# Kernel optimization log

Hardware: AMD Instinct MI355X
Metric: run time of the kernel (lower is better)

## Reference

```python
import jax, jax.numpy as jnp
import numpy as np

LN_EPS = 1e-5

# Per-tensor symmetric fake-quant (brevitas-style):
#  - activations: signed int8, non-narrow range [-128, 127], scale = absmax / 128
#  - weights:     signed int8, narrow range     [-127, 127], scale = absmax / 127

def _fake_quant(v, qmin, qmax, denom):
    s = jnp.max(jnp.abs(v)) / denom
    s = jnp.maximum(s, jnp.asarray(1e-12, v.dtype))
    q = jnp.clip(jnp.round(v / s), qmin, qmax)
    return q * s

def fq_act(v):
    return _fake_quant(v, -128.0, 127.0, 128.0)

def fq_weight(w):
    return _fake_quant(w, -127.0, 127.0, 127.0)

def layer_norm(x, gamma, beta):
    mu = jnp.mean(x, axis=-1, keepdims=True)
    var = jnp.mean(jnp.square(x - mu), axis=-1, keepdims=True)
    return (x - mu) * jax.lax.rsqrt(var + LN_EPS) * gamma + beta


def setup_inputs() -> dict:
    key = jax.random.key(0)
    k_x, k_w1, k_w2 = jax.random.split(key, 3)
    B, T, D, H = 16, 4096, 768, 3072
    x = jax.random.normal(k_x, (B, T, D), dtype=jnp.float32)
    gamma = jnp.ones((D,), jnp.float32)
    beta = jnp.zeros((D,), jnp.float32)
    W1 = jax.random.normal(k_w1, (H, D), dtype=jnp.float32) * (1.0 / np.sqrt(D))
    b1 = jnp.zeros((H,), jnp.float32)
    W2 = jax.random.normal(k_w2, (D, H), dtype=jnp.float32) * (1.0 / np.sqrt(H))
    b2 = jnp.zeros((D,), jnp.float32)
    return {"x": x, "gamma": gamma, "beta": beta, "W1": W1, "b1": b1, "W2": W2, "b2": b2}


def reference(x, gamma, beta, W1, b1, W2, b2):
    xn = layer_norm(x, gamma, beta)
    # fc1: quantize input + weight per-tensor, GEMM, float bias add
    h = jnp.einsum('btd,hd->bth', fq_act(xn), fq_weight(W1)) + b1
    h = jax.nn.gelu(h, approximate=False)  # nn.GELU default = exact erf
    # dropout p=0 -> identity
    out = jnp.einsum('bth,dh->btd', fq_act(h), fq_weight(W2)) + b2
    return out
```

## Files before the change

kernel.cpp:

```cpp
#include <hip/hip_runtime.h>
#include <math.h>


typedef __attribute__((ext_vector_type(4))) float  f4;
typedef __attribute__((ext_vector_type(4))) int    i32x4;
typedef __attribute__((ext_vector_type(4))) unsigned char  uc4;
typedef __attribute__((ext_vector_type(4))) unsigned int   u4;

__device__ __forceinline__ unsigned short f2bf_rn(float f) {
    unsigned u = __float_as_uint(f);
    u += 0x7FFFu + ((u >> 16) & 1u);
    return (unsigned short)(u >> 16);
}

template <int NW>
__device__ __forceinline__ void block_atomic_max(float v, unsigned* slot,
                                                 float* red, int tid) {
    int lane = tid & 63, wv = tid >> 6;
    #pragma unroll
    for (int m = 32; m; m >>= 1) v = fmaxf(v, __shfl_xor(v, m));
    if (lane == 0) red[wv] = v;
    __syncthreads();
    if (tid == 0) {
        float r = red[0];
        #pragma unroll
        for (int i = 1; i < NW; i++) r = fmaxf(r, red[i]);
        atomicMax(slot, __float_as_uint(r));
    }
}

__device__ __forceinline__ void gll16(const void* g, void* l) {
    __builtin_amdgcn_global_load_lds(
        (const __attribute__((address_space(1))) void*)g,
        (__attribute__((address_space(3))) void*)l, 16, 0, 0);
}

__device__ __forceinline__ void ln_row(const f4* xr, int lane, f4 v[3],
                                       float& mu, float& rs) {
    float s = 0.f;
    #pragma unroll
    for (int c = 0; c < 3; c++) {
        v[c] = xr[lane + 64 * c];
        s += v[c][0] + v[c][1] + v[c][2] + v[c][3];
    }
    #pragma unroll
    for (int m = 1; m < 64; m <<= 1) s += __shfl_xor(s, m);
    mu = s * (1.0f / 768.0f);
    float q = 0.f;
    #pragma unroll
    for (int c = 0; c < 3; c++) {
        #pragma unroll
        for (int k = 0; k < 4; k++) { float d = v[c][k] - mu; q += d * d; }
    }
    #pragma unroll
    for (int m = 1; m < 64; m <<= 1) q += __shfl_xor(q, m);
    rs = rsqrtf(q * (1.0f / 768.0f) + 1e-5f);
}

__global__ __launch_bounds__(256) void ln_absmax_kernel(
        const float* __restrict__ x, const float* __restrict__ gamma,
        const float* __restrict__ beta, unsigned* __restrict__ slot, long NR) {
    __shared__ float red[4];
    int tid = threadIdx.x, lane = tid & 63, wv = tid >> 6;
    const f4* g4 = (const f4*)gamma;
    const f4* b4 = (const f4*)beta;
    long rstep = (long)gridDim.x * 4;
    float wmax = 0.f;
    for (long row = (long)blockIdx.x * 4 + wv; row < NR; row += rstep) {
        const f4* xr = (const f4*)(x + row * 768);
        f4 v[3]; float mu, rs;
        ln_row(xr, lane, v, mu, rs);
        #pragma unroll
        for (int c = 0; c < 3; c++) {
            f4 g = g4[lane + 64 * c], b = b4[lane + 64 * c];
            #pragma unroll
            for (int k = 0; k < 4; k++) {
                float xn = (v[c][k] - mu) * rs * g[k] + b[k];
                wmax = fmaxf(wmax, fabsf(xn));
            }
        }
    }
    block_atomic_max<4>(wmax, slot, red, tid);
}

__global__ __launch_bounds__(256) void ln_quant_kernel(
        const float* __restrict__ x, const float* __restrict__ gamma,
        const float* __restrict__ beta, unsigned char* __restrict__ qx,
        const unsigned* __restrict__ amax_bits, long NR) {
    int tid = threadIdx.x, lane = tid & 63, wv = tid >> 6;
    long row = (long)blockIdx.x * 4 + wv;
    if (row >= NR) return;
    float sx = fmaxf(__uint_as_float(*amax_bits) * (1.0f / 128.0f), 1e-12f);
    const f4* xr = (const f4*)(x + row * 768);
    const f4* g4 = (const f4*)gamma;
    const f4* b4 = (const f4*)beta;
    f4 v[3]; float mu, rs;
    ln_row(xr, lane, v, mu, rs);
    uc4* qr = (uc4*)(qx + row * 768);
    #pragma unroll
    for (int c = 0; c < 3; c++) {
        f4 g = g4[lane + 64 * c], b = b4[lane + 64 * c];
        uc4 o;
        #pragma unroll
        for (int k = 0; k < 4; k++) {
            float xn = (v[c][k] - mu) * rs * g[k] + b[k];
            float q = fminf(fmaxf(rintf(xn / sx), -128.0f), 127.0f);
            o[k] = (unsigned char)(int)q;
        }
        qr[lane + 64 * c] = o;
    }
}

__global__ __launch_bounds__(256) void absmax_kernel(
        const float* __restrict__ w, long n4, unsigned* __restrict__ slot) {
    __shared__ float red[4];
    int tid = threadIdx.x;
    long stride = (long)gridDim.x * 256;
    float mx = 0.f;
    for (long i = (long)blockIdx.x * 256 + tid; i < n4; i += stride) {
        f4 v = ((const f4*)w)[i];
        mx = fmaxf(mx, fmaxf(fmaxf(fabsf(v[0]), fabsf(v[1])),
                             fmaxf(fabsf(v[2]), fabsf(v[3]))));
    }
    block_atomic_max<4>(mx, slot, red, tid);
}

__global__ __launch_bounds__(256) void quant_w_kernel(
        const float* __restrict__ w, unsigned char* __restrict__ qw, long n4,
        const unsigned* __restrict__ amax_bits) {
    long i = (long)blockIdx.x * 256 + threadIdx.x;
    if (i >= n4) return;
    float s = fmaxf(__uint_as_float(*amax_bits) * (1.0f / 127.0f), 1e-12f);
    f4 v = ((const f4*)w)[i];
    uc4 o;
    #pragma unroll
    for (int k = 0; k < 4; k++) {
        float q = fminf(fmaxf(rintf(v[k] / s), -127.0f), 127.0f);
        o[k] = (unsigned char)(int)q;
    }
    ((uc4*)qw)[i] = o;
}

__global__ __launch_bounds__(256) void quant_h_kernel(
        unsigned int* __restrict__ h, const unsigned* __restrict__ amax_bits,
        long n32) {
    long i = (long)blockIdx.x * 256 + threadIdx.x;
    if (i >= n32) return;
    float s = fmaxf(__uint_as_float(*amax_bits) * (1.0f / 128.0f), 1e-12f);
    u4 d0 = ((const u4*)h)[2 * i];
    u4 d1 = ((const u4*)h)[2 * i + 1];
    u4 o;
    #pragma unroll
    for (int w = 0; w < 4; w++) {
        unsigned r = 0;
        #pragma unroll
        for (int j = 0; j < 2; j++) {
            unsigned dw = (w < 2) ? d0[(w & 1) * 2 + j] : d1[(w & 1) * 2 + j];
            float lo = __uint_as_float(dw << 16);
            float hi = __uint_as_float(dw & 0xFFFF0000u);
            int qa = (int)fminf(fmaxf(rintf(lo / s), -128.0f), 127.0f);
            int qb = (int)fminf(fmaxf(rintf(hi / s), -128.0f), 127.0f);
            r |= ((unsigned)(unsigned char)qa) << (16 * j);
            r |= ((unsigned)(unsigned char)qb) << (16 * j + 8);
        }
        o[w] = r;
    }
    ((u4*)h)[2 * i] = o;
}

#define AB(b,kh) ((b)*65536 + (kh)*16384)
#define BB(b,kh) ((b)*65536 + 32768 + (kh)*16384)
#define VMC(n) asm volatile("s_waitcnt vmcnt(" #n ")" ::: "memory")
#define SK(eo, rbA, rbB) {                                                    \
    gll16(gA[0] + (long)(eo) * GAP, lds + (rbA) + ldst[0]);                   \
    gll16(gA[1] + (long)(eo) * GAP, lds + (rbA) + ldst[1]);                   \
    gll16(gB[0] + (eo),             lds + (rbB) + ldst[0]);                   \
    gll16(gB[1] + (eo),             lds + (rbB) + ldst[1]); }

#define PHASE2(BUF, KS, STAGE, TAIL) do {                                     \
    i32x4 aF[8]; i32x4 bF[4];                                                 \
    _Pragma("unroll")                                                         \
    for (int m_ = 0; m_ < 8; m_++)                                            \
      aF[m_] = *(const i32x4*)(lds + AB(BUF,KS) + aoff + m_ * 1024);          \
    _Pragma("unroll")                                                         \
    for (int n_ = 0; n_ < 4; n_++)                                            \
      bF[n_] = *(const i32x4*)(lds + BB(BUF,KS) + boff + n_ * 1024);          \
    STAGE                                                                     \
    __builtin_amdgcn_s_barrier();                                             \
    asm volatile("s_waitcnt lgkmcnt(0)" ::: "memory");                        \
    __builtin_amdgcn_s_setprio(1);                                            \
    _Pragma("unroll")                                                         \
    for (int m_ = 0; m_ < 8; m_++)                                            \
      _Pragma("unroll")                                                       \
      for (int n_ = 0; n_ < 4; n_++)                                          \
        acc[m_][n_] = __builtin_amdgcn_mfma_i32_16x16x64_i8(                  \
            aF[m_], bF[n_], acc[m_][n_], 0, 0, 0);                            \
    __builtin_amdgcn_s_setprio(0);                                            \
    TAIL                                                                      \
    __builtin_amdgcn_s_barrier();                                             \
  } while (0)

template <int GAP, int EPI>
__global__ __launch_bounds__(512, 2) void gemm256i(
        const unsigned char* __restrict__ A, const unsigned char* __restrict__ B,
        int K, const unsigned* __restrict__ amaxA_bits,
        const unsigned* __restrict__ amaxB_bits, const float* __restrict__ bias,
        void* __restrict__ Cout, int ldc, unsigned* __restrict__ amax_out) {
    __shared__ __align__(16) char lds[131072];
    __shared__ float red[8];
    int tid = threadIdx.x, lane = tid & 63, wv = tid >> 6;
    int wm = wv >> 2, wn = wv & 3;

    int nwg = gridDim.x * gridDim.y;
    int flat = blockIdx.y * gridDim.x + blockIdx.x;
    int swz = (flat & 7) * (nwg >> 3) + (flat >> 3);
    int ncol = gridDim.x;
    long rowBase = (long)(swz / ncol) * 256;
    long colBase = (long)(swz % ncol) * 256;

    i32x4 acc[8][4] = {};

    int rl = lane & 15, cq = lane >> 4;
    int roff = rl * 64 + ((cq ^ ((rl >> 1) & 3)) * 16);
    int aoff = wm * 8192 + roff;
    int boff = wn * 4096 + roff;

    const unsigned char* gA[2]; const unsigned char* gB[2]; int ldst[2];
    #pragma unroll
    for (int p = 0; p < 2; p++) {
        int s = p * 512 + tid;
        int r = s >> 2;
        int gc = (s & 3) ^ ((r >> 1) & 3);
        gA[p] = A + (rowBase + r) * (long)K * GAP + gc * 16 * GAP;
        gB[p] = B + (colBase + r) * (long)K + gc * 16;
        ldst[p] = s * 16;
    }

    SK(0,   AB(0,0), BB(0,0));
    SK(64,  AB(0,1), BB(0,1));
    SK(128, AB(1,0), BB(1,0));
    VMC(8);
    __builtin_amdgcn_s_barrier();

    const int nit = (K >> 8) - 1;
    for (int i = 0; i < nit; i++) {
        PHASE2(0,0, SK(192, AB(1,1), BB(1,1)), VMC(8); );
        PHASE2(0,1, SK(256, AB(0,0), BB(0,0)), VMC(8); );
        PHASE2(1,0, SK(320, AB(0,1), BB(0,1)), VMC(8); );
        PHASE2(1,1, SK(384, AB(1,0), BB(1,0)), VMC(8); );
        gA[0] += 256 * GAP; gA[1] += 256 * GAP; gB[0] += 256; gB[1] += 256;
    }
    PHASE2(0,0, SK(192, AB(1,1), BB(1,1)), VMC(8); );
    PHASE2(0,1, { },                       VMC(4); );
    PHASE2(1,0, { },                       VMC(0); );
    PHASE2(1,1, { },                               );

    float sA = fmaxf(__uint_as_float(*amaxA_bits) * (1.0f / 128.0f), 1e-12f);
    float sB = fmaxf(__uint_as_float(*amaxB_bits) * (1.0f / 127.0f), 1e-12f);
    float sAB = sA * sB;
    int cr = cq * 4;
    int cc = rl;

    float bv[4];
    #pragma unroll
    for (int n = 0; n < 4; n++) bv[n] = bias[colBase + wn * 64 + n * 16 + cc];

    if (EPI == 0) {
        unsigned short* Hm = (unsigned short*)Cout;
        float mx = 0.f;
        #pragma unroll
        for (int m = 0; m < 8; m++) {
            #pragma unroll
            for (int r = 0; r < 4; r++) {
                long ro = (rowBase + wm * 128 + m * 16 + cr + r) * (long)ldc
                          + colBase + wn * 64 + cc;
                #pragma unroll
                for (int n = 0; n < 4; n++) {
                    float v = (float)acc[m][n][r] * sAB + bv[n];
                    float g = 0.5f * v * (1.0f + erff(v * 0.70710678118654752f));
                    mx = fmaxf(mx, fabsf(g));
                    Hm[ro + n * 16] = f2bf_rn(g);
                }
            }
        }
        block_atomic_max<8>(mx, amax_out, red, tid);
    } else {
        float* O = (float*)Cout;
        #pragma unroll
        for (int m = 0; m < 8; m++) {
            #pragma unroll
            for (int r = 0; r < 4; r++) {
                long ro = (rowBase + wm * 128 + m * 16 + cr + r) * (long)ldc
                          + colBase + wn * 64 + cc;
                #pragma unroll
                for (int n = 0; n < 4; n++)
                    O[ro + n * 16] = (float)acc[m][n][r] * sAB + bv[n];
            }
        }
    }
}

extern "C" void kernel_launch(void* const* d_in, const int* in_sizes, int n_in,
                              void* d_out, int out_size, void* d_ws, size_t ws_size,
                              hipStream_t stream) {
    const float* x     = (const float*)d_in[0];
    const float* gamma = (const float*)d_in[1];
    const float* beta  = (const float*)d_in[2];
    const float* W1    = (const float*)d_in[3];
    const float* b1    = (const float*)d_in[4];
    const float* W2    = (const float*)d_in[5];
    const float* b2    = (const float*)d_in[6];
    float* out = (float*)d_out;

    const int  D  = in_sizes[1];
    const int  H  = in_sizes[4];
    const long NR = (long)in_sizes[0] / D;

    char* ws = (char*)d_ws;
    unsigned* amax = (unsigned*)ws;
    unsigned char* qx  = (unsigned char*)(ws + 256);
    unsigned char* qw1 = qx  + (size_t)NR * D;
    unsigned char* qw2 = qw1 + (size_t)H * D;
    unsigned short* hq = (unsigned short*)(qw2 + (size_t)H * D);

    hipMemsetAsync(amax, 0, 16, stream);

    long wn4 = (long)H * D / 4;
    absmax_kernel<<<1024, 256, 0, stream>>>(W1, wn4, amax + 1);
    absmax_kernel<<<1024, 256, 0, stream>>>(W2, wn4, amax + 2);
    ln_absmax_kernel<<<2048, 256, 0, stream>>>(x, gamma, beta, amax + 0, NR);

    quant_w_kernel<<<(unsigned)((wn4 + 255) / 256), 256, 0, stream>>>(W1, qw1, wn4, amax + 1);
    quant_w_kernel<<<(unsigned)((wn4 + 255) / 256), 256, 0, stream>>>(W2, qw2, wn4, amax + 2);
    ln_quant_kernel<<<(unsigned)(NR / 4), 256, 0, stream>>>(x, gamma, beta, qx, amax + 0, NR);

    dim3 g1(H / 256, (unsigned)(NR / 256));
    gemm256i<1, 0><<<g1, 512, 0, stream>>>(qx, qw1, D, amax + 0, amax + 1, b1,
                                           (void*)hq, H, amax + 3);

    long n32 = NR * (long)H / 16;
    quant_h_kernel<<<(unsigned)((n32 + 255) / 256), 256, 0, stream>>>(
        (unsigned int*)hq, amax + 3, n32);

    dim3 g2(D / 256, (unsigned)(NR / 256));
    gemm256i<2, 1><<<g2, 512, 0, stream>>>((const unsigned char*)hq, qw2, H,
                                           amax + 3, amax + 2, b2,
                                           (void*)out, D, nullptr);
}
```

Baseline: 1.201 ms.

## Shrink GEMM tile to 128x256 with triple-buffered pipeline and fast erf

Both int8 GEMMs move from a 256x256 output tile with a 2-buffer, 2-subphase K pipeline to a 128x256 tile with a 3-stage ring of 64-wide K slices. LDS use falls from 128 KB to 72 KB and the accumulators are halved, with launch bounds raised to 4 blocks per CU to allow higher occupancy. The GELU epilogue replaces libm erff with an Abramowitz-Stegun polynomial using a hardware reciprocal and fast exp, which cuts epilogue cost but adds approximation error near the bf16/int8 quantization steps. Smaller tiles also mean more A/B reloads per output element.

```diff
diff --git a/kernel.cpp b/kernel.cpp
--- a/kernel.cpp
+++ b/kernel.cpp
@@ -11,6 +11,20 @@
     unsigned u = __float_as_uint(f);
     u += 0x7FFFu + ((u >> 16) & 1u);
     return (unsigned short)(u >> 16);
+}
+
+__device__ __forceinline__ float erf_fast(float x) {
+    float ax = fabsf(x);
+    float t = __builtin_amdgcn_rcpf(fmaf(0.3275911f, ax, 1.0f));
+    float y = t * (0.254829592f +
+              t * (-0.284496736f +
+              t * (1.421413741f +
+              t * (-1.453152027f +
+              t * 1.061405429f))));
+    float e = __expf(-ax * ax);
+    float r = fmaf(-y, e, 1.0f);
+    unsigned s = __float_as_uint(x) & 0x80000000u;
+    return __uint_as_float(__float_as_uint(r) | s);
 }
 
 template <int NW>
@@ -168,29 +182,28 @@
     ((u4*)h)[2 * i] = o;
 }
 
-#define AB(b,kh) ((b)*65536 + (kh)*16384)
-#define BB(b,kh) ((b)*65536 + 32768 + (kh)*16384)
+#define AB3(b) ((b)*24576)
+#define BB3(b) ((b)*24576 + 8192)
 #define VMC(n) asm volatile("s_waitcnt vmcnt(" #n ")" ::: "memory")
-#define SK(eo, rbA, rbB) {                                                    \
-    gll16(gA[0] + (long)(eo) * GAP, lds + (rbA) + ldst[0]);                   \
-    gll16(gA[1] + (long)(eo) * GAP, lds + (rbA) + ldst[1]);                   \
-    gll16(gB[0] + (eo),             lds + (rbB) + ldst[0]);                   \
-    gll16(gB[1] + (eo),             lds + (rbB) + ldst[1]); }
-
-#define PHASE2(BUF, KS, STAGE, TAIL) do {                                     \
-    i32x4 aF[8]; i32x4 bF[4];                                                 \
+#define SK3(eo, b) {                                                          \
+    gll16(gA0 + (long)(eo) * GAP, lds + AB3(b) + ldstA);                      \
+    gll16(gB0 + (eo),             lds + BB3(b) + ldstB);                      \
+    gll16(gB1 + (eo),             lds + BB3(b) + 8192 + ldstB); }
+
+#define PH3(b, STAGE, TAIL) do {                                              \
+    i32x4 aF[4]; i32x4 bF[4];                                                 \
     _Pragma("unroll")                                                         \
-    for (int m_ = 0; m_ < 8; m_++)                                            \
-      aF[m_] = *(const i32x4*)(lds + AB(BUF,KS) + aoff + m_ * 1024);          \
+    for (int m_ = 0; m_ < 4; m_++)                                            \
+      aF[m_] = *(const i32x4*)(lds + AB3(b) + aoff + m_ * 1024);              \
     _Pragma("unroll")                                                         \
     for (int n_ = 0; n_ < 4; n_++)                                            \
-      bF[n_] = *(const i32x4*)(lds + BB(BUF,KS) + boff + n_ * 1024);          \
+      bF[n_] = *(const i32x4*)(lds + BB3(b) + boff + n_ * 1024);              \
     STAGE                                                                     \
     __builtin_amdgcn_s_barrier();                                             \
     asm volatile("s_waitcnt lgkmcnt(0)" ::: "memory");                        \
     __builtin_amdgcn_s_setprio(1);                                            \
     _Pragma("unroll")                                                         \
-    for (int m_ = 0; m_ < 8; m_++)                                            \
+    for (int m_ = 0; m_ < 4; m_++)                                            \
       _Pragma("unroll")                                                       \
       for (int n_ = 0; n_ < 4; n_++)                                          \
         acc[m_][n_] = __builtin_amdgcn_mfma_i32_16x16x64_i8(                  \
@@ -201,13 +214,12 @@
   } while (0)
 
 template <int GAP, int EPI>
-__global__ __launch_bounds__(512, 2) void gemm256i(
+__global__ __launch_bounds__(512, 4) void gemm128i(
         const unsigned char* __restrict__ A, const unsigned char* __restrict__ B,
         int K, const unsigned* __restrict__ amaxA_bits,
         const unsigned* __restrict__ amaxB_bits, const float* __restrict__ bias,
         void* __restrict__ Cout, int ldc, unsigned* __restrict__ amax_out) {
-    __shared__ __align__(16) char lds[131072];
-    __shared__ float red[8];
+    __shared__ __align__(16) char lds[73728];
     int tid = threadIdx.x, lane = tid & 63, wv = tid >> 6;
     int wm = wv >> 2, wn = wv & 3;
 
@@ -215,45 +227,41 @@
     int flat = blockIdx.y * gridDim.x + blockIdx.x;
     int swz = (flat & 7) * (nwg >> 3) + (flat >> 3);
     int ncol = gridDim.x;
-    long rowBase = (long)(swz / ncol) * 256;
+    long rowBase = (long)(swz / ncol) * 128;
     long colBase = (long)(swz % ncol) * 256;
 
-    i32x4 acc[8][4] = {};
+    i32x4 acc[4][4] = {};
 
     int rl = lane & 15, cq = lane >> 4;
     int roff = rl * 64 + ((cq ^ ((rl >> 1) & 3)) * 16);
-    int aoff = wm * 8192 + roff;
+    int aoff = wm * 4096 + roff;
     int boff = wn * 4096 + roff;
 
-    const unsigned char* gA[2]; const unsigned char* gB[2]; int ldst[2];
-    #pragma unroll
-    for (int p = 0; p < 2; p++) {
-        int s = p * 512 + tid;
-        int r = s >> 2;
-        int gc = (s & 3) ^ ((r >> 1) & 3);
-        gA[p] = A + (rowBase + r) * (long)K * GAP + gc * 16 * GAP;
-        gB[p] = B + (colBase + r) * (long)K + gc * 16;
-        ldst[p] = s * 16;
-    }
-
-    SK(0,   AB(0,0), BB(0,0));
-    SK(64,  AB(0,1), BB(0,1));
-    SK(128, AB(1,0), BB(1,0));
-    VMC(8);
+    int rA = tid >> 2;
+    int gcA = (tid & 3) ^ ((rA >> 1) & 3);
+    const unsigned char* gA0 = A + (rowBase + rA) * (long)K * GAP + gcA * 16 * GAP;
+    int s1 = 512 + tid;
+    int rB1 = s1 >> 2;
+    int gcB1 = (s1 & 3) ^ ((rB1 >> 1) & 3);
+    const unsigned char* gB0 = B + (colBase + rA) * (long)K + gcA * 16;
+    const unsigned char* gB1 = B + (colBase + rB1) * (long)K + gcB1 * 16;
+    int ldstA = tid * 16, ldstB = tid * 16;
+
+    SK3(0, 0);
+    SK3(64, 1);
+    VMC(3);
     __builtin_amdgcn_s_barrier();
 
-    const int nit = (K >> 8) - 1;
-    for (int i = 0; i < nit; i++) {
-        PHASE2(0,0, SK(192, AB(1,1), BB(1,1)), VMC(8); );
-        PHASE2(0,1, SK(256, AB(0,0), BB(0,0)), VMC(8); );
-        PHASE2(1,0, SK(320, AB(0,1), BB(0,1)), VMC(8); );
-        PHASE2(1,1, SK(384, AB(1,0), BB(1,0)), VMC(8); );
-        gA[0] += 256 * GAP; gA[1] += 256 * GAP; gB[0] += 256; gB[1] += 256;
-    }
-    PHASE2(0,0, SK(192, AB(1,1), BB(1,1)), VMC(8); );
-    PHASE2(0,1, { },                       VMC(4); );
-    PHASE2(1,0, { },                       VMC(0); );
-    PHASE2(1,1, { },                               );
+    const int n3 = (K / 64 - 3) / 3;
+    for (int i = 0; i < n3; i++) {
+        PH3(0, SK3(128, 2), VMC(3); );
+        PH3(1, SK3(192, 0), VMC(3); );
+        PH3(2, SK3(256, 1), VMC(3); );
+        gA0 += 192 * GAP; gB0 += 192; gB1 += 192;
+    }
+    PH3(0, SK3(128, 2), VMC(3); );
+    PH3(1, { },         VMC(0); );
+    PH3(2, { },                  );
 
     float sA = fmaxf(__uint_as_float(*amaxA_bits) * (1.0f / 128.0f), 1e-12f);
     float sB = fmaxf(__uint_as_float(*amaxB_bits) * (1.0f / 127.0f), 1e-12f);
@@ -269,28 +277,29 @@
         unsigned short* Hm = (unsigned short*)Cout;
         float mx = 0.f;
         #pragma unroll
-        for (int m = 0; m < 8; m++) {
+        for (int m = 0; m < 4; m++) {
             #pragma unroll
             for (int r = 0; r < 4; r++) {
-                long ro = (rowBase + wm * 128 + m * 16 + cr + r) * (long)ldc
+                long ro = (rowBase + wm * 64 + m * 16 + cr + r) * (long)ldc
                           + colBase + wn * 64 + cc;
                 #pragma unroll
                 for (int n = 0; n < 4; n++) {
                     float v = (float)acc[m][n][r] * sAB + bv[n];
-                    float g = 0.5f * v * (1.0f + erff(v * 0.70710678118654752f));
+                    float g = 0.5f * v *
+                              (1.0f + erf_fast(v * 0.70710678118654752f));
                     mx = fmaxf(mx, fabsf(g));
                     Hm[ro + n * 16] = f2bf_rn(g);
                 }
             }
         }
-        block_atomic_max<8>(mx, amax_out, red, tid);
+        block_atomic_max<8>(mx, amax_out, (float*)lds, tid);
     } else {
         float* O = (float*)Cout;
         #pragma unroll
-        for (int m = 0; m < 8; m++) {
+        for (int m = 0; m < 4; m++) {
             #pragma unroll
             for (int r = 0; r < 4; r++) {
-                long ro = (rowBase + wm * 128 + m * 16 + cr + r) * (long)ldc
+                long ro = (rowBase + wm * 64 + m * 16 + cr + r) * (long)ldc
                           + colBase + wn * 64 + cc;
                 #pragma unroll
                 for (int n = 0; n < 4; n++)
@@ -334,16 +343,16 @@
     quant_w_kernel<<<(unsigned)((wn4 + 255) / 256), 256, 0, stream>>>(W2, qw2, wn4, amax + 2);
     ln_quant_kernel<<<(unsigned)(NR / 4), 256, 0, stream>>>(x, gamma, beta, qx, amax + 0, NR);
 
-    dim3 g1(H / 256, (unsigned)(NR / 256));
-    gemm256i<1, 0><<<g1, 512, 0, stream>>>(qx, qw1, D, amax + 0, amax + 1, b1,
+    dim3 g1(H / 256, (unsigned)(NR / 128));
+    gemm128i<1, 0><<<g1, 512, 0, stream>>>(qx, qw1, D, amax + 0, amax + 1, b1,
                                            (void*)hq, H, amax + 3);
 
     long n32 = NR * (long)H / 16;
     quant_h_kernel<<<(unsigned)((n32 + 255) / 256), 256, 0, stream>>>(
         (unsigned int*)hq, amax + 3, n32);
 
-    dim3 g2(D / 256, (unsigned)(NR / 256));
-    gemm256i<2, 1><<<g2, 512, 0, stream>>>((const unsigned char*)hq, qw2, H,
+    dim3 g2(D / 256, (unsigned)(NR / 128));
+    gemm128i<2, 1><<<g2, 512, 0, stream>>>((const unsigned char*)hq, qw2, H,
                                            amax + 3, amax + 2, b2,
                                            (void*)out, D, nullptr);
 }
```

Result: faster. 1.070 ms (-10.9%).
